# Optimization experiments

Hardware: AMD Instinct MI355X
Metric: run time of the kernel (lower is better)

## Reference

```python
import jax, jax.numpy as jnp
import numpy as np

B, S, H, D = 8, 4096, 32, 128
DM = H * D

def setup_inputs() -> dict:
    key = jax.random.key(0)
    k1, k2, k3, k4, k5 = jax.random.split(key, 5)
    return {
        "hidden_state": jax.random.normal(k1, (B, DM), dtype=jnp.float32),
        "key_states": jax.random.normal(k2, (B, S, DM), dtype=jnp.float32),
        "value_states": jax.random.normal(k3, (B, S, DM), dtype=jnp.float32),
        "Wq": jax.random.normal(k4, (DM, DM), dtype=jnp.float32) * 0.02,
        "bq": jax.random.normal(k5, (DM,), dtype=jnp.float32) * 0.02,
    }

def reference(hidden_state, key_states, value_states, Wq, bq):
    # q projection: torch Linear -> x @ W^T + b
    q = (hidden_state @ Wq.T + bq).reshape(B, H, D)          # [B,H,D]
    k = key_states.reshape(B, S, H, D)                        # [B,S,H,D]
    v = value_states.reshape(B, S, H, D)
    # NOTE: original module applies no 1/sqrt(D) scaling
    scores = jnp.einsum('bhd,bshd->bhs', q, k)                # [B,H,S]
    probs = jax.nn.softmax(scores, axis=-1)
    out = jnp.einsum('bhs,bshd->bhd', probs, v)               # [B,H,D]
    return out[:, :, None, :]                                 # [B,H,1,D] to match torch output
```

## Files before the change

### kernel.cpp

```cpp
#include <hip/hip_runtime.h>

#define B 8
#define S 4096
#define H 32
#define D 128
#define DM 4096

#define NT 1024
#define WAVES 16

typedef float v4f __attribute__((ext_vector_type(4)));

__global__ __launch_bounds__(256) void qproj_kernel(
    const float* __restrict__ hidden, const float* __restrict__ Wq,
    const float* __restrict__ bq, float* __restrict__ qout)
{
    const int lane = threadIdx.x & 63;
    const int wave = threadIdx.x >> 6;
    const int j0 = (blockIdx.x * 4 + wave) * 2;
    const int j1 = j0 + 1;

    const v4f* __restrict__ w0 = (const v4f*)(Wq + (size_t)j0 * DM);
    const v4f* __restrict__ w1 = (const v4f*)(Wq + (size_t)j1 * DM);
    const v4f* __restrict__ hid = (const v4f*)hidden;

    float a0[B], a1[B];
#pragma unroll
    for (int b = 0; b < B; ++b) { a0[b] = 0.f; a1[b] = 0.f; }

#pragma unroll 4
    for (int i = 0; i < DM / (4 * 64); ++i) {
        const int idx = lane + 64 * i;
        const v4f wv0 = __builtin_nontemporal_load(w0 + idx);
        const v4f wv1 = __builtin_nontemporal_load(w1 + idx);
#pragma unroll
        for (int b = 0; b < B; ++b) {
            const v4f hv = hid[b * (DM / 4) + idx];
            a0[b] += wv0[0] * hv[0] + wv0[1] * hv[1] + wv0[2] * hv[2] + wv0[3] * hv[3];
            a1[b] += wv1[0] * hv[0] + wv1[1] * hv[1] + wv1[2] * hv[2] + wv1[3] * hv[3];
        }
    }
#pragma unroll
    for (int b = 0; b < B; ++b) {
#pragma unroll
        for (int mk = 1; mk <= 32; mk <<= 1) {
            a0[b] += __shfl_xor(a0[b], mk);
            a1[b] += __shfl_xor(a1[b], mk);
        }
    }
    if (lane == 0) {
        const float bias0 = bq[j0];
        const float bias1 = bq[j1];
#pragma unroll
        for (int b = 0; b < B; ++b) {
            qout[b * DM + j0] = a0[b] + bias0;
            qout[b * DM + j1] = a1[b] + bias1;
        }
    }
}

__global__ __launch_bounds__(NT) void attn_kernel(
    const float* __restrict__ kptr, const float* __restrict__ vptr,
    const float* __restrict__ qws, float* __restrict__ out)
{
    __shared__ float sc[S];
    __shared__ float red[WAVES];
    __shared__ float outp[WAVES][D];

    const int tid  = threadIdx.x;
    const int lane = tid & 63;
    const int wave = tid >> 6;
    const int g    = lane >> 5;
    const int l    = lane & 31;
    const int b    = blockIdx.x >> 5;
    const int h    = blockIdx.x & (H - 1);

    const size_t base = ((size_t)b * S * H + h) * D;
    const float* kb = kptr + base;
    const float* vb = vptr + base;

    const v4f q4 = *(const v4f*)(qws + (size_t)b * DM + h * D + 4 * l);

#pragma unroll 2
    for (int it = 0; it < S / 32; ++it) {
        const int s = it * 32 + 2 * wave + g;
        const v4f k4 = __builtin_nontemporal_load(
            (const v4f*)(kb + (size_t)s * DM + 4 * l));
        float p = q4[0] * k4[0] + q4[1] * k4[1] + q4[2] * k4[2] + q4[3] * k4[3];
        p += __shfl_xor(p, 16);
        p += __shfl_xor(p, 8);
        p += __shfl_xor(p, 4);
        p += __shfl_xor(p, 2);
        p += __shfl_xor(p, 1);
        if (l == 0) sc[s] = p;
    }
    __syncthreads();

    float m = -3.4e38f;
    for (int i = tid; i < S; i += NT) m = fmaxf(m, sc[i]);
#pragma unroll
    for (int mk = 1; mk <= 32; mk <<= 1) m = fmaxf(m, __shfl_xor(m, mk));
    if (lane == 0) red[wave] = m;
    __syncthreads();
    float M = red[0];
#pragma unroll
    for (int w = 1; w < WAVES; ++w) M = fmaxf(M, red[w]);

    float lsum = 0.f;
    for (int i = tid; i < S; i += NT) {
        const float e = __expf(sc[i] - M);
        sc[i] = e;
        lsum += e;
    }
#pragma unroll
    for (int mk = 1; mk <= 32; mk <<= 1) lsum += __shfl_xor(lsum, mk);
    __syncthreads();
    if (lane == 0) red[wave] = lsum;
    __syncthreads();
    float tot = 0.f;
#pragma unroll
    for (int w = 0; w < WAVES; ++w) tot += red[w];
    const float inv = 1.0f / tot;

    v4f acc = {0.f, 0.f, 0.f, 0.f};
    const int s0 = wave * (S / WAVES);
#pragma unroll 2
    for (int i = 0; i < S / WAVES; i += 2) {
        const int s = s0 + i + g;
        const float p = sc[s];
        const v4f v4 = __builtin_nontemporal_load(
            (const v4f*)(vb + (size_t)s * DM + 4 * l));
        acc[0] += p * v4[0];
        acc[1] += p * v4[1];
        acc[2] += p * v4[2];
        acc[3] += p * v4[3];
    }
    acc[0] += __shfl_xor(acc[0], 32);
    acc[1] += __shfl_xor(acc[1], 32);
    acc[2] += __shfl_xor(acc[2], 32);
    acc[3] += __shfl_xor(acc[3], 32);
    if (g == 0) *(v4f*)(&outp[wave][4 * l]) = acc;
    __syncthreads();

    if (tid < D) {
        float r = 0.f;
#pragma unroll
        for (int w = 0; w < WAVES; ++w) r += outp[w][tid];
        out[(size_t)(b * H + h) * D + tid] = r * inv;
    }
}

extern "C" void kernel_launch(void* const* d_in, const int* in_sizes, int n_in,
                              void* d_out, int out_size, void* d_ws, size_t ws_size,
                              hipStream_t stream)
{
    const float* hidden = (const float*)d_in[0];
    const float* keys   = (const float*)d_in[1];
    const float* vals   = (const float*)d_in[2];
    const float* Wq     = (const float*)d_in[3];
    const float* bq     = (const float*)d_in[4];
    float* outp = (float*)d_out;
    float* qws  = (float*)d_ws;

    qproj_kernel<<<DM / 8, 256, 0, stream>>>(hidden, Wq, bq, qws);
    attn_kernel<<<B * H, NT, 0, stream>>>(keys, vals, qws, outp);
}
```

Before: 217.8 us.

## Split attention over sequence chunks with 4-head blocks and a combine kernel

```diff
diff --git a/kernel.cpp b/kernel.cpp
--- a/kernel.cpp
+++ b/kernel.cpp
@@ -6,8 +6,14 @@
 #define D 128
 #define DM 4096
 
+#define SPLIT 4
+#define NR (S / SPLIT)
+#define HQ 4
+#define NHQ (H / HQ)
 #define NT 1024
 #define WAVES 16
+#define RPW (NR / WAVES)
+#define PSTR 132
 
 typedef float v4f __attribute__((ext_vector_type(4)));
 
@@ -59,95 +65,133 @@
     }
 }
 
-__global__ __launch_bounds__(NT) void attn_kernel(
+__global__ __launch_bounds__(NT) void attn_partial(
     const float* __restrict__ kptr, const float* __restrict__ vptr,
-    const float* __restrict__ qws, float* __restrict__ out)
-{
-    __shared__ float sc[S];
-    __shared__ float red[WAVES];
-    __shared__ float outp[WAVES][D];
+    const float* __restrict__ qws, float* __restrict__ part)
+{
+    __shared__ float sc[HQ][NR];
+    __shared__ float outp[WAVES][HQ][D];
+    __shared__ float redM[HQ][4];
+    __shared__ float redS[HQ][4];
 
     const int tid  = threadIdx.x;
     const int lane = tid & 63;
-    const int wave = tid >> 6;
-    const int g    = lane >> 5;
-    const int l    = lane & 31;
+    const int w    = tid >> 6;
+    const int half = lane >> 5;
+    const int c    = blockIdx.x & (SPLIT - 1);
+    const int hq   = (blockIdx.x >> 2) & (NHQ - 1);
     const int b    = blockIdx.x >> 5;
-    const int h    = blockIdx.x & (H - 1);
-
-    const size_t base = ((size_t)b * S * H + h) * D;
-    const float* kb = kptr + base;
-    const float* vb = vptr + base;
-
-    const v4f q4 = *(const v4f*)(qws + (size_t)b * DM + h * D + 4 * l);
-
-#pragma unroll 2
-    for (int it = 0; it < S / 32; ++it) {
-        const int s = it * 32 + 2 * wave + g;
-        const v4f k4 = __builtin_nontemporal_load(
-            (const v4f*)(kb + (size_t)s * DM + 4 * l));
-        float p = q4[0] * k4[0] + q4[1] * k4[1] + q4[2] * k4[2] + q4[3] * k4[3];
-        p += __shfl_xor(p, 16);
-        p += __shfl_xor(p, 8);
-        p += __shfl_xor(p, 4);
-        p += __shfl_xor(p, 2);
-        p += __shfl_xor(p, 1);
-        if (l == 0) sc[s] = p;
-    }
-    __syncthreads();
-
+
+    const size_t rowbase = ((size_t)b * S + (size_t)c * NR) * DM + hq * (HQ * D);
+    const float* kq = kptr + rowbase;
+    const float* vq = vptr + rowbase;
+
+    const v4f qA = *(const v4f*)(qws + (size_t)b * DM + hq * (HQ * D) + 4 * lane);
+    const v4f qB = *(const v4f*)(qws + (size_t)b * DM + hq * (HQ * D) + 256 + 4 * lane);
+
+    const int s0 = w * RPW;
+
+#pragma unroll 4
+    for (int i = 0; i < RPW; ++i) {
+        const int s = s0 + i;
+        const v4f kA = __builtin_nontemporal_load(
+            (const v4f*)(kq + (size_t)s * DM + 4 * lane));
+        const v4f kB = __builtin_nontemporal_load(
+            (const v4f*)(kq + (size_t)s * DM + 256 + 4 * lane));
+        float pA = qA[0]*kA[0] + qA[1]*kA[1] + qA[2]*kA[2] + qA[3]*kA[3];
+        float pB = qB[0]*kB[0] + qB[1]*kB[1] + qB[2]*kB[2] + qB[3]*kB[3];
+#pragma unroll
+        for (int mk = 1; mk <= 16; mk <<= 1) {
+            pA += __shfl_xor(pA, mk);
+            pB += __shfl_xor(pB, mk);
+        }
+        if ((lane & 31) == 0) {
+            sc[half][s]     = pA;
+            sc[2 + half][s] = pB;
+        }
+    }
+    __syncthreads();
+
+    const int qh = tid >> 8;
+    const int qt = tid & 255;
     float m = -3.4e38f;
-    for (int i = tid; i < S; i += NT) m = fmaxf(m, sc[i]);
+#pragma unroll
+    for (int j = 0; j < NR / 256; ++j) m = fmaxf(m, sc[qh][qt + 256 * j]);
 #pragma unroll
     for (int mk = 1; mk <= 32; mk <<= 1) m = fmaxf(m, __shfl_xor(m, mk));
-    if (lane == 0) red[wave] = m;
-    __syncthreads();
-    float M = red[0];
-#pragma unroll
-    for (int w = 1; w < WAVES; ++w) M = fmaxf(M, red[w]);
-
+    if (lane == 0) redM[qh][w & 3] = m;
+    __syncthreads();
+    const float M = fmaxf(fmaxf(redM[qh][0], redM[qh][1]),
+                          fmaxf(redM[qh][2], redM[qh][3]));
     float lsum = 0.f;
-    for (int i = tid; i < S; i += NT) {
-        const float e = __expf(sc[i] - M);
-        sc[i] = e;
+#pragma unroll
+    for (int j = 0; j < NR / 256; ++j) {
+        const int i = qt + 256 * j;
+        const float e = __expf(sc[qh][i] - M);
+        sc[qh][i] = e;
         lsum += e;
     }
 #pragma unroll
     for (int mk = 1; mk <= 32; mk <<= 1) lsum += __shfl_xor(lsum, mk);
-    __syncthreads();
-    if (lane == 0) red[wave] = lsum;
-    __syncthreads();
-    float tot = 0.f;
-#pragma unroll
-    for (int w = 0; w < WAVES; ++w) tot += red[w];
-    const float inv = 1.0f / tot;
-
-    v4f acc = {0.f, 0.f, 0.f, 0.f};
-    const int s0 = wave * (S / WAVES);
-#pragma unroll 2
-    for (int i = 0; i < S / WAVES; i += 2) {
-        const int s = s0 + i + g;
-        const float p = sc[s];
-        const v4f v4 = __builtin_nontemporal_load(
-            (const v4f*)(vb + (size_t)s * DM + 4 * l));
-        acc[0] += p * v4[0];
-        acc[1] += p * v4[1];
-        acc[2] += p * v4[2];
-        acc[3] += p * v4[3];
-    }
-    acc[0] += __shfl_xor(acc[0], 32);
-    acc[1] += __shfl_xor(acc[1], 32);
-    acc[2] += __shfl_xor(acc[2], 32);
-    acc[3] += __shfl_xor(acc[3], 32);
-    if (g == 0) *(v4f*)(&outp[wave][4 * l]) = acc;
-    __syncthreads();
-
-    if (tid < D) {
+    if (lane == 0) redS[qh][w & 3] = lsum;
+    __syncthreads();
+
+    v4f accA = {0.f, 0.f, 0.f, 0.f};
+    v4f accB = {0.f, 0.f, 0.f, 0.f};
+#pragma unroll 4
+    for (int i = 0; i < RPW; ++i) {
+        const int s = s0 + i;
+        const float pA = sc[half][s];
+        const float pB = sc[2 + half][s];
+        const v4f vA = __builtin_nontemporal_load(
+            (const v4f*)(vq + (size_t)s * DM + 4 * lane));
+        const v4f vB = __builtin_nontemporal_load(
+            (const v4f*)(vq + (size_t)s * DM + 256 + 4 * lane));
+        accA[0] += pA * vA[0]; accA[1] += pA * vA[1];
+        accA[2] += pA * vA[2]; accA[3] += pA * vA[3];
+        accB[0] += pB * vB[0]; accB[1] += pB * vB[1];
+        accB[2] += pB * vB[2]; accB[3] += pB * vB[3];
+    }
+    *(v4f*)(&outp[w][half][4 * (lane & 31)])     = accA;
+    *(v4f*)(&outp[w][2 + half][4 * (lane & 31)]) = accB;
+    __syncthreads();
+
+    if (tid < HQ * D) {
+        const int hd = tid >> 7;
+        const int d  = tid & 127;
         float r = 0.f;
 #pragma unroll
-        for (int w = 0; w < WAVES; ++w) r += outp[w][tid];
-        out[(size_t)(b * H + h) * D + tid] = r * inv;
-    }
+        for (int ww = 0; ww < WAVES; ++ww) r += outp[ww][hd][d];
+        float* rec = part + ((size_t)(b * H + hq * HQ + hd) * SPLIT + c) * PSTR;
+        rec[d] = r;
+        if (d == 0) {
+            const float Mh = fmaxf(fmaxf(redM[hd][0], redM[hd][1]),
+                                   fmaxf(redM[hd][2], redM[hd][3]));
+            const float Sh = redS[hd][0] + redS[hd][1] + redS[hd][2] + redS[hd][3];
+            rec[D] = Mh;
+            rec[D + 1] = Sh;
+        }
+    }
+}
+
+__global__ __launch_bounds__(128) void combine_kernel(
+    const float* __restrict__ part, float* __restrict__ out)
+{
+    const int bh = blockIdx.x;
+    const int d  = threadIdx.x;
+    const float* rec = part + (size_t)bh * SPLIT * PSTR;
+
+    float M = -3.4e38f;
+#pragma unroll
+    for (int c = 0; c < SPLIT; ++c) M = fmaxf(M, rec[c * PSTR + D]);
+    float denom = 0.f, o = 0.f;
+#pragma unroll
+    for (int c = 0; c < SPLIT; ++c) {
+        const float wgt = __expf(rec[c * PSTR + D] - M);
+        denom += wgt * rec[c * PSTR + D + 1];
+        o     += wgt * rec[c * PSTR + d];
+    }
+    out[(size_t)bh * D + d] = o / denom;
 }
 
 extern "C" void kernel_launch(void* const* d_in, const int* in_sizes, int n_in,
@@ -161,7 +205,9 @@
     const float* bq     = (const float*)d_in[4];
     float* outp = (float*)d_out;
     float* qws  = (float*)d_ws;
+    float* part = qws + (size_t)B * DM;
 
     qproj_kernel<<<DM / 8, 256, 0, stream>>>(hidden, Wq, bq, qws);
-    attn_kernel<<<B * H, NT, 0, stream>>>(keys, vals, qws, outp);
-}
+    attn_partial<<<B * NHQ * SPLIT, NT, 0, stream>>>(keys, vals, qws, part);
+    combine_kernel<<<B * H, 128, 0, stream>>>(part, outp);
+}
```

Result: slower. 230.5 us (+5.8%).
